# Kernel optimization log

Hardware: AMD Instinct MI355X
Metric: run time of the kernel (lower is better)

Reference implementation:

```python
import jax, jax.numpy as jnp
import numpy as np

B, NP, P, DIM = 128, 64, 128, 512
DST, DCONV, DEPTH = 16, 4, 2
DIN = 2 * DIM          # expand * dim
DTR = DIM // 16        # dt_rank
NCLS = 32


def setup_inputs() -> dict:
    key = jax.random.key(0)
    ks = jax.random.split(key, 12)
    r = lambda k, shape, s=0.02: jax.random.normal(k, shape, jnp.float32) * s
    A_log = jnp.log(jnp.arange(1, DST + 1, dtype=jnp.float32))  # S4D-real init
    return {
        "series": jax.random.normal(ks[0], (B, NP * P), jnp.float32),
        "seg_w": r(ks[1], (NP, P, DIM)),
        "seg_b": jnp.zeros((NP, DIM), jnp.float32),
        "ln_g": jnp.ones((NP, DIM), jnp.float32),
        "ln_b": jnp.zeros((NP, DIM), jnp.float32),
        "in_proj_w": r(ks[2], (DEPTH, 2 * DIN, DIM)),
        "conv_w": r(ks[3], (DEPTH, DIN, DCONV), 0.1),
        "conv_b": jnp.zeros((DEPTH, DIN), jnp.float32),
        "x_proj_w": r(ks[4], (DEPTH, DTR + 2 * DST, DIN)),
        "dt_proj_w": r(ks[5], (DEPTH, DIN, DTR), 0.1),
        "dt_proj_b": r(ks[6], (DEPTH, DIN), 0.5) - 4.0,  # small softplus(dt)
        "A_log": jnp.tile(A_log, (DEPTH, DIN, 1)),
        "D": jnp.ones((DEPTH, DIN), jnp.float32),
        "out_proj_w": r(ks[7], (DEPTH, DIM, DIN)),
        "head_ln_g": jnp.ones((NP * DIM,), jnp.float32),
        "head_ln_b": jnp.zeros((NP * DIM,), jnp.float32),
        "head_w": r(ks[8], (NCLS, NP * DIM)),
        "head_b": jnp.zeros((NCLS,), jnp.float32),
    }


def _layernorm(x, g, b, eps=1e-5):
    mu = x.mean(-1, keepdims=True)
    var = x.var(-1, keepdims=True)
    return (x - mu) / jnp.sqrt(var + eps) * g + b


def _mamba_block(x, wi, cw, cb, wx, wdt, bdt, A_log, Dp, wo):
    # x: [b, l, DIM]
    b, l, _ = x.shape
    xz = jnp.einsum('bld,ed->ble', x, wi)            # [b, l, 2*DIN]
    u, z = jnp.split(xz, 2, axis=-1)
    # depthwise causal conv1d (kernel DCONV, left pad DCONV-1)
    up = jnp.pad(u, ((0, 0), (DCONV - 1, 0), (0, 0)))
    uc = sum(up[:, k:k + l, :] * cw[:, k] for k in range(DCONV)) + cb
    uc = jax.nn.silu(uc)
    x_dbl = jnp.einsum('bld,ed->ble', uc, wx)        # [b, l, DTR+2*DST]
    dt, Bm, Cm = jnp.split(x_dbl, [DTR, DTR + DST], axis=-1)
    delta = jax.nn.softplus(jnp.einsum('blr,dr->bld', dt, wdt) + bdt)  # [b,l,DIN]
    A = -jnp.exp(A_log)                               # [DIN, DST]

    def step(h, inp):
        d_t, B_t, C_t, u_t = inp                      # [b,DIN],[b,DST],[b,DST],[b,DIN]
        dA = jnp.exp(d_t[:, :, None] * A)             # [b, DIN, DST]
        h = dA * h + (d_t * u_t)[:, :, None] * B_t[:, None, :]
        y = jnp.einsum('bdn,bn->bd', h, C_t)
        return h, y

    xs = (delta.transpose(1, 0, 2), Bm.transpose(1, 0, 2),
          Cm.transpose(1, 0, 2), uc.transpose(1, 0, 2))
    h0 = jnp.zeros((b, DIN, DST), x.dtype)
    _, ys = jax.lax.scan(step, h0, xs)                # [l, b, DIN]
    y = ys.transpose(1, 0, 2) + uc * Dp
    y = y * jax.nn.silu(z)
    return jnp.einsum('bld,ed->ble', y, wo)           # [b, l, DIM]


def _forward(series, seg_w, seg_b, ln_g, ln_b, in_proj_w, conv_w, conv_b,
             x_proj_w, dt_proj_w, dt_proj_b, A_log, D, out_proj_w,
             head_ln_g, head_ln_b, head_w, head_b):
    b = series.shape[0]
    x = series.reshape(b, NP, P)                      # equal-size pathway split
    x = jnp.einsum('bnp,npd->bnd', x, seg_w) + seg_b  # per-pathway Linear
    x = _layernorm(x, ln_g, ln_b)                     # per-pathway LayerNorm
    for i in range(DEPTH):                            # stacked Mamba (no residual)
        x = _mamba_block(x, in_proj_w[i], conv_w[i], conv_b[i], x_proj_w[i],
                         dt_proj_w[i], dt_proj_b[i], A_log[i], D[i], out_proj_w[i])
    x = x.reshape(b, NP * DIM)
    x = _layernorm(x, head_ln_g, head_ln_b)
    return x @ head_w.T + head_b


def reference(series, seg_w, seg_b, ln_g, ln_b, in_proj_w, conv_w, conv_b,
              x_proj_w, dt_proj_w, dt_proj_b, A_log, D, out_proj_w,
              head_ln_g, head_ln_b, head_w, head_b):
    return _forward(series, seg_w, seg_b, ln_g, ln_b, in_proj_w, conv_w, conv_b,
                    x_proj_w, dt_proj_w, dt_proj_b, A_log, D, out_proj_w,
                    head_ln_g, head_ln_b, head_w, head_b)
```

## Files before the change

### kernel.cpp

```cpp
#include <hip/hip_runtime.h>

typedef unsigned short u16;
typedef unsigned int   u32;
typedef __attribute__((ext_vector_type(8))) short short8;
typedef __attribute__((ext_vector_type(4))) float floatx4;

static __device__ __forceinline__ float silu_f(float x){
  return x / (1.f + __expf(-x));
}
static __device__ __forceinline__ float bfu2f(u16 u){
  union { u32 i; float f; } v; v.i = ((u32)u) << 16; return v.f;
}
static __device__ __forceinline__ u16 f2bfu(float f){
  union { float f; u32 i; } v; v.f = f;
  u32 x = v.i;
  u32 r = (x + 0x7fffu + ((x >> 16) & 1u)) >> 16;
  return (u16)r;
}
static __device__ __forceinline__ float softplus_f(float v){
  return fmaxf(v, 0.f) + log1pf(__expf(-fabsf(v)));
}

constexpr int cB = 128, cNP = 64, cP = 128, cDIM = 512, cDIN = 1024;
constexpr int cDST = 16, cDTR = 32, cNCLS = 32;
constexpr int cBL = cB * cNP;
constexpr int cXZ = 2 * cDIN;

__global__ __launch_bounds__(256) void k_f2bf(
    const float* __restrict__ src, u16* __restrict__ dst)
{
  const int i = (blockIdx.x * 256 + threadIdx.x) * 4;
  float4 v = *(const float4*)(src + i);
  ushort4 o;
  o.x = f2bfu(v.x); o.y = f2bfu(v.y); o.z = f2bfu(v.z); o.w = f2bfu(v.w);
  *(ushort4*)(dst + i) = o;
}

__global__ __launch_bounds__(256) void k_segT(
    const float* __restrict__ src, u16* __restrict__ dst)
{
  const int n = blockIdx.z;
  const int p0 = blockIdx.x * 32;
  const int d0 = blockIdx.y * 32;
  const int tx = threadIdx.x & 31;
  const int ty = threadIdx.x >> 5;
  __shared__ float t[32][33];
#pragma unroll
  for (int r = 0; r < 4; ++r)
    t[ty + r * 8][tx] = src[(size_t)n * (cP * cDIM) + (p0 + ty + r * 8) * cDIM + d0 + tx];
  __syncthreads();
#pragma unroll
  for (int r = 0; r < 4; ++r)
    dst[(size_t)n * (cDIM * cP) + (d0 + ty + r * 8) * cP + p0 + tx] =
        f2bfu(t[tx][ty + r * 8]);
}

template<bool AF32, int EPI>
__global__ __launch_bounds__(256) void k_gemm_mfma(
    const void* __restrict__ Av, int lda,
    const u16* __restrict__ W,
    float* __restrict__ C, int ldc,
    u16* __restrict__ Cb, int ldcb,
    const float* __restrict__ bias,
    int K, long azs, long wzs, long czs)
{
  constexpr int LDT = 40;
  __shared__ __align__(16) u16 As[128 * LDT];
  __shared__ __align__(16) u16 Ws[128 * LDT];

  const int bz = blockIdx.z;
  const u16* Wz = W + (size_t)bz * wzs;

  const int tid = threadIdx.x;
  const int bm = blockIdx.x * 128;
  const int bn = blockIdx.y * 128;
  const int wave = tid >> 6;
  const int lane = tid & 63;
  const int wm = (wave & 1) * 64;
  const int wn = (wave >> 1) * 64;
  const int l15 = lane & 15;
  const int quad = lane >> 4;

  floatx4 acc[4][4];
#pragma unroll
  for (int i = 0; i < 4; ++i)
#pragma unroll
    for (int j = 0; j < 4; ++j) acc[i][j] = (floatx4){0.f, 0.f, 0.f, 0.f};

  const int r0 = tid >> 2;
  const int c0 = (tid & 3) * 8;

  const float* Af = (const float*)Av + (AF32 ? (size_t)bz * azs : 0);
  const u16*   Ab = (const u16*)Av + (AF32 ? 0 : (size_t)bz * azs);

  float4 fa0, fb0, fa1, fb1;
  short8 ra0, ra1, rw0, rw1;

  if constexpr (AF32) {
    const float* p0 = Af + (size_t)(bm + r0) * lda + c0;
    const float* p1 = Af + (size_t)(bm + r0 + 64) * lda + c0;
    fa0 = *(const float4*)p0; fb0 = *(const float4*)(p0 + 4);
    fa1 = *(const float4*)p1; fb1 = *(const float4*)(p1 + 4);
  } else {
    ra0 = *(const short8*)(Ab + (size_t)(bm + r0)      * lda + c0);
    ra1 = *(const short8*)(Ab + (size_t)(bm + r0 + 64) * lda + c0);
  }
  rw0 = *(const short8*)(Wz + (size_t)(bn + r0)      * K + c0);
  rw1 = *(const short8*)(Wz + (size_t)(bn + r0 + 64) * K + c0);

  for (int k0 = 0; k0 < K; k0 += 32) {
    if constexpr (AF32) {
      short8 s0, s1;
      s0[0] = (short)f2bfu(fa0.x); s0[1] = (short)f2bfu(fa0.y);
      s0[2] = (short)f2bfu(fa0.z); s0[3] = (short)f2bfu(fa0.w);
      s0[4] = (short)f2bfu(fb0.x); s0[5] = (short)f2bfu(fb0.y);
      s0[6] = (short)f2bfu(fb0.z); s0[7] = (short)f2bfu(fb0.w);
      s1[0] = (short)f2bfu(fa1.x); s1[1] = (short)f2bfu(fa1.y);
      s1[2] = (short)f2bfu(fa1.z); s1[3] = (short)f2bfu(fa1.w);
      s1[4] = (short)f2bfu(fb1.x); s1[5] = (short)f2bfu(fb1.y);
      s1[6] = (short)f2bfu(fb1.z); s1[7] = (short)f2bfu(fb1.w);
      *(short8*)&As[r0 * LDT + c0] = s0;
      *(short8*)&As[(r0 + 64) * LDT + c0] = s1;
    } else {
      *(short8*)&As[r0 * LDT + c0] = ra0;
      *(short8*)&As[(r0 + 64) * LDT + c0] = ra1;
    }
    *(short8*)&Ws[r0 * LDT + c0] = rw0;
    *(short8*)&Ws[(r0 + 64) * LDT + c0] = rw1;
    __syncthreads();

    const int kn = k0 + 32;
    if (kn < K) {
      if constexpr (AF32) {
        const float* p0 = Af + (size_t)(bm + r0) * lda + kn + c0;
        const float* p1 = Af + (size_t)(bm + r0 + 64) * lda + kn + c0;
        fa0 = *(const float4*)p0; fb0 = *(const float4*)(p0 + 4);
        fa1 = *(const float4*)p1; fb1 = *(const float4*)(p1 + 4);
      } else {
        ra0 = *(const short8*)(Ab + (size_t)(bm + r0)      * lda + kn + c0);
        ra1 = *(const short8*)(Ab + (size_t)(bm + r0 + 64) * lda + kn + c0);
      }
      rw0 = *(const short8*)(Wz + (size_t)(bn + r0)      * K + kn + c0);
      rw1 = *(const short8*)(Wz + (size_t)(bn + r0 + 64) * K + kn + c0);
    }

    short8 af[4], bf[4];
#pragma unroll
    for (int i = 0; i < 4; ++i)
      af[i] = *(const short8*)&As[(wm + i * 16 + l15) * LDT + quad * 8];
#pragma unroll
    for (int j = 0; j < 4; ++j)
      bf[j] = *(const short8*)&Ws[(wn + j * 16 + l15) * LDT + quad * 8];
#pragma unroll
    for (int i = 0; i < 4; ++i)
#pragma unroll
      for (int j = 0; j < 4; ++j)
        acc[i][j] = __builtin_amdgcn_mfma_f32_16x16x32_bf16(
            af[i], bf[j], acc[i][j], 0, 0, 0);
    __syncthreads();
  }

#pragma unroll
  for (int i = 0; i < 4; ++i) {
    const int m0 = bm + wm + i * 16 + quad * 4;
#pragma unroll
    for (int j = 0; j < 4; ++j) {
      const int n = bn + wn + j * 16 + l15;
      if constexpr (EPI == 1) {
        const float bs = bias[n];
#pragma unroll
        for (int r = 0; r < 4; ++r)
          Cb[(size_t)(m0 + r) * ldcb + n + bz * czs] =
              f2bfu(softplus_f(acc[i][j][r] + bs));
      } else {
        if (C) {
#pragma unroll
          for (int r = 0; r < 4; ++r)
            C[(size_t)(m0 + r) * ldc + n + bz * czs] = acc[i][j][r];
        }
        if (Cb) {
#pragma unroll
          for (int r = 0; r < 4; ++r)
            Cb[(size_t)(m0 + r) * ldcb + n + bz * czs] = f2bfu(acc[i][j][r]);
        }
      }
    }
  }
}

__global__ __launch_bounds__(256) void k_ln(
    const float* __restrict__ xs, const float* __restrict__ sb,
    const float* __restrict__ ln_g, const float* __restrict__ ln_b,
    u16* __restrict__ x0b)
{
  const int tid = threadIdx.x;
  const int r = blockIdx.x * 4 + (tid >> 6);
  const int lane = tid & 63;
  const int d = lane * 8;
  const int n = r & 63;

  const float* row = xs + (size_t)r * cDIM + d;
  float4 a = *(const float4*)row;
  float4 b = *(const float4*)(row + 4);
  const float* sbp = sb + n * cDIM + d;
  float4 s0 = *(const float4*)sbp;
  float4 s1 = *(const float4*)(sbp + 4);
  a.x += s0.x; a.y += s0.y; a.z += s0.z; a.w += s0.w;
  b.x += s1.x; b.y += s1.y; b.z += s1.z; b.w += s1.w;

  float s  = a.x + a.y + a.z + a.w + b.x + b.y + b.z + b.w;
  float s2 = a.x*a.x + a.y*a.y + a.z*a.z + a.w*a.w
           + b.x*b.x + b.y*b.y + b.z*b.z + b.w*b.w;
#pragma unroll
  for (int m = 1; m < 64; m <<= 1) {
    s  += __shfl_xor(s,  m, 64);
    s2 += __shfl_xor(s2, m, 64);
  }
  const float mu = s * (1.f / cDIM);
  const float var = s2 * (1.f / cDIM) - mu * mu;
  const float rstd = rsqrtf(var + 1e-5f);

  const float* g = ln_g + n * cDIM + d;
  const float* be = ln_b + n * cDIM + d;
  float4 g0 = *(const float4*)g, g1 = *(const float4*)(g + 4);
  float4 b0 = *(const float4*)be, b1 = *(const float4*)(be + 4);
  ushort4 o0, o1;
  o0.x = f2bfu((a.x - mu) * rstd * g0.x + b0.x);
  o0.y = f2bfu((a.y - mu) * rstd * g0.y + b0.y);
  o0.z = f2bfu((a.z - mu) * rstd * g0.z + b0.z);
  o0.w = f2bfu((a.w - mu) * rstd * g0.w + b0.w);
  o1.x = f2bfu((b.x - mu) * rstd * g1.x + b1.x);
  o1.y = f2bfu((b.y - mu) * rstd * g1.y + b1.y);
  o1.z = f2bfu((b.z - mu) * rstd * g1.z + b1.z);
  o1.w = f2bfu((b.w - mu) * rstd * g1.w + b1.w);
  *(ushort4*)(x0b + (size_t)r * cDIM + d) = o0;
  *(ushort4*)(x0b + (size_t)r * cDIM + d + 4) = o1;
}

__global__ __launch_bounds__(256) void k_conv(
    const u16* __restrict__ xz16, const float* __restrict__ cw,
    const float* __restrict__ cb, u16* __restrict__ uc)
{
  const int t = blockIdx.x * 256 + threadIdx.x;
  const int b = t >> 10;
  const int d = t & 1023;
  const float w0 = cw[d * 4 + 0], w1 = cw[d * 4 + 1];
  const float w2 = cw[d * 4 + 2], w3 = cw[d * 4 + 3];
  const float bias = cb[d];
  const u16* src = xz16 + (size_t)b * cNP * cXZ + d;
  u16* dst = uc + (size_t)b * cNP * cDIN + d;

  float u0 = 0.f, u1 = 0.f, u2 = 0.f;
  float cur[8];
#pragma unroll
  for (int i = 0; i < 8; ++i) cur[i] = bfu2f(src[(size_t)i * cXZ]);

  for (int c = 0; c < 8; ++c) {
    float nxt[8];
    if (c < 7) {
#pragma unroll
      for (int i = 0; i < 8; ++i)
        nxt[i] = bfu2f(src[(size_t)((c + 1) * 8 + i) * cXZ]);
    }
    u16 o[8];
#pragma unroll
    for (int i = 0; i < 8; ++i) {
      float v = w0 * u0 + w1 * u1 + w2 * u2 + w3 * cur[i] + bias;
      o[i] = f2bfu(silu_f(v));
      u0 = u1; u1 = u2; u2 = cur[i];
    }
#pragma unroll
    for (int i = 0; i < 8; ++i) dst[(size_t)(c * 8 + i) * cDIN] = o[i];
    if (c < 7) {
#pragma unroll
      for (int i = 0; i < 8; ++i) cur[i] = nxt[i];
    }
  }
}

__global__ __launch_bounds__(128) void k_xproj(
    const u16* __restrict__ A, const u16* __restrict__ W,
    float* __restrict__ xpart)
{
  constexpr int LDT = 40;
  __shared__ __align__(16) u16 As[128 * LDT];
  __shared__ __align__(16) u16 Ws[64 * LDT];

  const int tid = threadIdx.x;
  const int bm = blockIdx.x * 128;
  const int kbase = blockIdx.y * 256;
  const int wave = tid >> 6;
  const int lane = tid & 63;
  const int wm = wave * 64;
  const int l15 = lane & 15;
  const int quad = lane >> 4;

  floatx4 acc[4][4];
#pragma unroll
  for (int i = 0; i < 4; ++i)
#pragma unroll
    for (int j = 0; j < 4; ++j) acc[i][j] = (floatx4){0.f, 0.f, 0.f, 0.f};

  short8 rA[4], rW[2];
#pragma unroll
  for (int it = 0; it < 4; ++it) {
    int idx = tid + it * 128, row = idx >> 2, cc = (idx & 3) * 8;
    rA[it] = *(const short8*)(A + (size_t)(bm + row) * cDIN + kbase + cc);
  }
#pragma unroll
  for (int it = 0; it < 2; ++it) {
    int idx = tid + it * 128, row = idx >> 2, cc = (idx & 3) * 8;
    rW[it] = *(const short8*)(W + (size_t)row * cDIN + kbase + cc);
  }

  for (int kk = 0; kk < 256; kk += 32) {
#pragma unroll
    for (int it = 0; it < 4; ++it) {
      int idx = tid + it * 128, row = idx >> 2, cc = (idx & 3) * 8;
      *(short8*)&As[row * LDT + cc] = rA[it];
    }
#pragma unroll
    for (int it = 0; it < 2; ++it) {
      int idx = tid + it * 128, row = idx >> 2, cc = (idx & 3) * 8;
      *(short8*)&Ws[row * LDT + cc] = rW[it];
    }
    __syncthreads();

    if (kk + 32 < 256) {
      const int k0 = kbase + kk + 32;
#pragma unroll
      for (int it = 0; it < 4; ++it) {
        int idx = tid + it * 128, row = idx >> 2, cc = (idx & 3) * 8;
        rA[it] = *(const short8*)(A + (size_t)(bm + row) * cDIN + k0 + cc);
      }
#pragma unroll
      for (int it = 0; it < 2; ++it) {
        int idx = tid + it * 128, row = idx >> 2, cc = (idx & 3) * 8;
        rW[it] = *(const short8*)(W + (size_t)row * cDIN + k0 + cc);
      }
    }

    short8 af[4], bf[4];
#pragma unroll
    for (int i = 0; i < 4; ++i)
      af[i] = *(const short8*)&As[(wm + i * 16 + l15) * LDT + quad * 8];
#pragma unroll
    for (int j = 0; j < 4; ++j)
      bf[j] = *(const short8*)&Ws[(j * 16 + l15) * LDT + quad * 8];
#pragma unroll
    for (int i = 0; i < 4; ++i)
#pragma unroll
      for (int j = 0; j < 4; ++j)
        acc[i][j] = __builtin_amdgcn_mfma_f32_16x16x32_bf16(
            af[i], bf[j], acc[i][j], 0, 0, 0);
    __syncthreads();
  }

  float* out = xpart + (size_t)blockIdx.y * cBL * 64;
#pragma unroll
  for (int i = 0; i < 4; ++i) {
    const int m0 = bm + wm + i * 16 + quad * 4;
#pragma unroll
    for (int j = 0; j < 4; ++j) {
      const int n = j * 16 + l15;
#pragma unroll
      for (int r = 0; r < 4; ++r)
        out[(size_t)(m0 + r) * 64 + n] = acc[i][j][r];
    }
  }
}

__global__ __launch_bounds__(256) void k_xred(
    const float* __restrict__ xpart, float* __restrict__ C,
    u16* __restrict__ Cb)
{
  const int i = (blockIdx.x * 256 + threadIdx.x) * 4;
  float4 s = *(const float4*)(xpart + i);
#pragma unroll
  for (int k = 1; k < 4; ++k) {
    float4 v = *(const float4*)(xpart + (size_t)k * cBL * 64 + i);
    s.x += v.x; s.y += v.y; s.z += v.z; s.w += v.w;
  }
  *(float4*)(C + i) = s;
  ushort4 o;
  o.x = f2bfu(s.x); o.y = f2bfu(s.y); o.z = f2bfu(s.z); o.w = f2bfu(s.w);
  *(ushort4*)(Cb + i) = o;
}

__global__ __launch_bounds__(256) void k_scan(
    const u16* __restrict__ xz16, u16* __restrict__ uc,
    const float* __restrict__ xdbl, const float* __restrict__ A_log,
    const float* __restrict__ Dp)
{
  const int b = blockIdx.x;
  const int tid = threadIdx.x;
  const int d = blockIdx.y * 256 + tid;

  __shared__ float sBC[cNP][32];
  {
    const float4* src = (const float4*)xdbl;
    for (int i = tid; i < cNP * 8; i += 256) {
      int l = i >> 3, q = i & 7;
      *(float4*)&sBC[l][q * 4] = src[(size_t)(b * cNP + l) * 16 + 8 + q];
    }
  }

  float A[cDST];
  {
    const float4* ap = (const float4*)(A_log + (size_t)d * cDST);
#pragma unroll
    for (int q = 0; q < 4; ++q) {
      float4 w = ap[q];
      A[q*4+0] = -__expf(w.x); A[q*4+1] = -__expf(w.y);
      A[q*4+2] = -__expf(w.z); A[q*4+3] = -__expf(w.w);
    }
  }
  float h[cDST];
#pragma unroll
  for (int n = 0; n < cDST; ++n) h[n] = 0.f;
  const float Dv = Dp[d];
  __syncthreads();

  const u16* dsrc = xz16 + d;
  const u16* zsrc = xz16 + cDIN + d;
  u16* usrc = uc + d;
  const size_t rb = (size_t)b * cNP;

  float dvc[8], zvc[8], uvc[8];
#pragma unroll
  for (int i = 0; i < 8; ++i) {
    dvc[i] = bfu2f(dsrc[(rb + i) * cXZ]);
    zvc[i] = bfu2f(zsrc[(rb + i) * cXZ]);
    uvc[i] = bfu2f(usrc[(rb + i) * cDIN]);
  }

  for (int c = 0; c < 8; ++c) {
    float dvn[8], zvn[8], uvn[8];
    if (c < 7) {
#pragma unroll
      for (int i = 0; i < 8; ++i) {
        const size_t row = rb + (c + 1) * 8 + i;
        dvn[i] = bfu2f(dsrc[row * cXZ]);
        zvn[i] = bfu2f(zsrc[row * cXZ]);
        uvn[i] = bfu2f(usrc[row * cDIN]);
      }
    }
    u16 yo[8];
#pragma unroll
    for (int i = 0; i < 8; ++i) {
      const int l = c * 8 + i;
      const float dv = dvc[i], zv = zvc[i], uv = uvc[i];
      const float du = dv * uv;
      float y = 0.f;
#pragma unroll
      for (int n = 0; n < cDST; ++n) {
        float dA = __expf(dv * A[n]);
        h[n] = dA * h[n] + du * sBC[l][n];
        y += h[n] * sBC[l][16 + n];
      }
      y = (y + uv * Dv) * silu_f(zv);
      yo[i] = f2bfu(y);
    }
#pragma unroll
    for (int i = 0; i < 8; ++i)
      usrc[(rb + c * 8 + i) * cDIN] = yo[i];
    if (c < 7) {
#pragma unroll
      for (int i = 0; i < 8; ++i) {
        dvc[i] = dvn[i]; zvc[i] = zvn[i]; uvc[i] = uvn[i];
      }
    }
  }
}

__global__ __launch_bounds__(256) void k_hstats1(
    const float* __restrict__ x, float* __restrict__ pst)
{
  const int b = blockIdx.x;
  const int chunk = blockIdx.y;
  const int tid = threadIdx.x;
  const float4* r4 = (const float4*)(x + (size_t)b * (cNP * cDIM) + chunk * 4096);
  float4 v = r4[tid];
  float4 w = r4[tid + 256];
  float4 u = r4[tid + 512];
  float4 t = r4[tid + 768];
  float s  = v.x + v.y + v.z + v.w + w.x + w.y + w.z + w.w
           + u.x + u.y + u.z + u.w + t.x + t.y + t.z + t.w;
  float s2 = v.x*v.x + v.y*v.y + v.z*v.z + v.w*v.w
           + w.x*w.x + w.y*w.y + w.z*w.z + w.w*w.w
           + u.x*u.x + u.y*u.y + u.z*u.z + u.w*u.w
           + t.x*t.x + t.y*t.y + t.z*t.z + t.w*t.w;
  __shared__ float red[512];
  red[tid] = s; red[256 + tid] = s2;
  __syncthreads();
  for (int st = 128; st > 0; st >>= 1) {
    if (tid < st) { red[tid] += red[tid + st]; red[256+tid] += red[256+tid+st]; }
    __syncthreads();
  }
  if (tid == 0) {
    pst[(b * 8 + chunk) * 2]     = red[0];
    pst[(b * 8 + chunk) * 2 + 1] = red[256];
  }
}

__global__ __launch_bounds__(128) void k_hstats2(
    const float* __restrict__ pst, float* __restrict__ stats)
{
  const int b = threadIdx.x;
  float s = 0.f, s2 = 0.f;
#pragma unroll
  for (int c = 0; c < 8; ++c) {
    s  += pst[(b * 8 + c) * 2];
    s2 += pst[(b * 8 + c) * 2 + 1];
  }
  const float mu = s * (1.f / (cNP * cDIM));
  const float var = s2 * (1.f / (cNP * cDIM)) - mu * mu;
  stats[2 * b]     = mu;
  stats[2 * b + 1] = rsqrtf(var + 1e-5f);
}

__global__ __launch_bounds__(256) void k_head1(
    const float* __restrict__ x, const float* __restrict__ stats,
    const float* __restrict__ hg, const float* __restrict__ hb,
    const u16* __restrict__ hwb, float* __restrict__ hpart)
{
  const int b = blockIdx.x;
  const int chunk = blockIdx.y;
  const int tid = threadIdx.x;
  const float mu = stats[2 * b], rstd = stats[2 * b + 1];
  const float* row = x + (size_t)b * (cNP * cDIM);
  const int k0 = chunk * 2048;

  float acc[cNCLS];
#pragma unroll
  for (int c = 0; c < cNCLS; ++c) acc[c] = 0.f;

#pragma unroll
  for (int it = 0; it < 4; ++it) {
    const int i0 = k0 + it * 512 + tid * 2;
    float xn0 = (row[i0]     - mu) * rstd * hg[i0]     + hb[i0];
    float xn1 = (row[i0 + 1] - mu) * rstd * hg[i0 + 1] + hb[i0 + 1];
#pragma unroll
    for (int c = 0; c < cNCLS; ++c) {
      u32 w2 = *(const u32*)(hwb + (size_t)c * (cNP * cDIM) + i0);
      acc[c] += xn0 * bfu2f((u16)(w2 & 0xffffu)) + xn1 * bfu2f((u16)(w2 >> 16));
    }
  }

  __shared__ float sred[cNCLS * 257];
#pragma unroll
  for (int c = 0; c < cNCLS; ++c) sred[c * 257 + tid] = acc[c];
  __syncthreads();
  if (tid < cNCLS * 8) {
    const int c = tid >> 3, p = tid & 7;
    float s = 0.f;
#pragma unroll
    for (int i = 0; i < 32; ++i) s += sred[c * 257 + p * 32 + i];
    s += __shfl_xor(s, 1, 64);
    s += __shfl_xor(s, 2, 64);
    s += __shfl_xor(s, 4, 64);
    if (p == 0) hpart[(size_t)(b * 16 + chunk) * cNCLS + c] = s;
  }
}

__global__ __launch_bounds__(64) void k_head2(
    const float* __restrict__ hpart, const float* __restrict__ hbias,
    float* __restrict__ out)
{
  const int b = blockIdx.x;
  const int c = threadIdx.x;
  if (c < cNCLS) {
    float s = 0.f;
#pragma unroll
    for (int k = 0; k < 16; ++k)
      s += hpart[(size_t)(b * 16 + k) * cNCLS + c];
    out[b * cNCLS + c] = s + hbias[c];
  }
}

extern "C" void kernel_launch(void* const* d_in, const int* in_sizes, int n_in,
                              void* d_out, int out_size, void* d_ws, size_t ws_size,
                              hipStream_t stream)
{
  (void)in_sizes; (void)n_in; (void)out_size; (void)ws_size;

  const float* series    = (const float*)d_in[0];
  const float* seg_w     = (const float*)d_in[1];
  const float* seg_b     = (const float*)d_in[2];
  const float* ln_g      = (const float*)d_in[3];
  const float* ln_b      = (const float*)d_in[4];
  const float* in_proj_w = (const float*)d_in[5];
  const float* conv_w    = (const float*)d_in[6];
  const float* conv_b    = (const float*)d_in[7];
  const float* x_proj_w  = (const float*)d_in[8];
  const float* dt_proj_w = (const float*)d_in[9];
  const float* dt_proj_b = (const float*)d_in[10];
  const float* A_log     = (const float*)d_in[11];
  const float* Dp        = (const float*)d_in[12];
  const float* out_proj_w= (const float*)d_in[13];
  const float* head_ln_g = (const float*)d_in[14];
  const float* head_ln_b = (const float*)d_in[15];
  const float* head_w    = (const float*)d_in[16];
  const float* head_b    = (const float*)d_in[17];

  u16*   xz16   = (u16*)d_ws;
  float* x0     = (float*)(xz16 + (size_t)cBL * cXZ);
  float* xsegf  = x0;
  float* xdbl   = x0 + (size_t)cBL * cDIM;
  float* stats  = xdbl + (size_t)cBL * 64;
  float* pst    = stats + 256;
  float* hpart  = pst + 128 * 8 * 2;
  u16*   x0b    = (u16*)(hpart + 128 * 16 * 32);
  u16*   wib    = x0b + (size_t)cBL * cDIM;
  u16*   wob    = wib + (size_t)2 * (2*cDIN) * cDIM;
  u16*   wdtb   = wob + (size_t)2 * cDIM * cDIN;
  u16*   wxb    = wdtb + (size_t)2 * cDIN * cDTR;
  u16*   xdbl16 = wxb + (size_t)2 * 64 * cDIN;
  u16*   wsegT  = xdbl16 + (size_t)cBL * 64;
  u16*   ucb16  = wsegT + (size_t)cNP * cDIM * cP;
  u16*   hwb    = ucb16 + (size_t)cBL * cDIN;
  float* xpart  = (float*)x0b;

  k_f2bf<<<(2 * (2*cDIN) * cDIM) / 1024, 256, 0, stream>>>(in_proj_w, wib);
  k_f2bf<<<(2 * cDIM * cDIN) / 1024, 256, 0, stream>>>(out_proj_w, wob);
  k_f2bf<<<(2 * cDIN * cDTR) / 1024, 256, 0, stream>>>(dt_proj_w, wdtb);
  k_f2bf<<<(2 * 64 * cDIN) / 1024, 256, 0, stream>>>(x_proj_w, wxb);
  k_f2bf<<<(cNCLS * cNP * cDIM) / 1024, 256, 0, stream>>>(head_w, hwb);
  k_segT<<<dim3(cP/32, cDIM/32, cNP), 256, 0, stream>>>(seg_w, wsegT);

  k_gemm_mfma<true,0><<<dim3(1, cDIM/128, cNP), 256, 0, stream>>>(
      series, cNP * cP, wsegT, xsegf, cNP * cDIM, (u16*)nullptr, 0,
      nullptr, cP, (long)cP, (long)cDIM * cP, (long)cDIM);
  k_ln<<<cBL / 4, 256, 0, stream>>>(xsegf, seg_b, ln_g, ln_b, x0b);

  for (int dep = 0; dep < 2; ++dep) {
    const u16*   wi  = wib  + (size_t)dep * (2*cDIN) * cDIM;
    const u16*   wo  = wob  + (size_t)dep * cDIM * cDIN;
    const u16*   wdt = wdtb + (size_t)dep * cDIN * cDTR;
    const u16*   wx  = wxb  + (size_t)dep * 64 * cDIN;
    const float* cwd = conv_w     + (size_t)dep * cDIN * 4;
    const float* cbd = conv_b     + (size_t)dep * cDIN;
    const float* bdt = dt_proj_b  + (size_t)dep * cDIN;
    const float* Ald = A_log      + (size_t)dep * cDIN * cDST;
    const float* Dd  = Dp         + (size_t)dep * cDIN;

    k_gemm_mfma<false,0><<<dim3(cBL/128, (2*cDIN)/128), 256, 0, stream>>>(
        x0b, cDIM, wi, (float*)nullptr, 0, xz16, cXZ, nullptr, cDIM, 0, 0, 0);
    k_conv<<<(cB * cDIN) / 256, 256, 0, stream>>>(xz16, cwd, cbd, ucb16);
    k_xproj<<<dim3(cBL / 128, 4), 128, 0, stream>>>(ucb16, wx, xpart);
    k_xred<<<(cBL * 64) / 1024, 256, 0, stream>>>(xpart, xdbl, xdbl16);
    k_gemm_mfma<false,1><<<dim3(cBL/128, cDIN/128), 256, 0, stream>>>(
        xdbl16, 64, wdt, (float*)nullptr, 0, xz16, cXZ, bdt, cDTR, 0, 0, 0);
    k_scan<<<dim3(cB, 4), 256, 0, stream>>>(xz16, ucb16, xdbl, Ald, Dd);
    k_gemm_mfma<false,0><<<dim3(cBL/128, cDIM/128), 256, 0, stream>>>(
        ucb16, cDIN, wo,
        dep ? x0 : (float*)nullptr, cDIM,
        dep ? (u16*)nullptr : x0b, cDIM,
        nullptr, cDIN, 0, 0, 0);
  }

  k_hstats1<<<dim3(cB, 8), 256, 0, stream>>>(x0, pst);
  k_hstats2<<<1, 128, 0, stream>>>(pst, stats);
  k_head1<<<dim3(cB, 16), 256, 0, stream>>>(x0, stats, head_ln_g, head_ln_b,
                                            hwb, hpart);
  k_head2<<<cB, 64, 0, stream>>>(hpart, head_b, (float*)d_out);
}
```

Baseline: 438.6 us.

## Fuse causal conv into in_proj GEMM epilogue and use geometric exp in scan

The in_proj GEMM gains an epilogue mode that stages the u half of each tile in LDS and applies the depthwise causal conv plus SiLU directly, removing the separate conv kernel and its global read of u. The scan kernel detects at runtime whether A follows the S4D-real geometric pattern and, if so, replaces 16 exponentials per step with one exp and repeated multiplication. The fused epilogue adds 32KB of shared memory per block, which may cut occupancy. The power chain adds small rounding drift compared with computing each exp directly.

```diff
diff --git a/kernel.cpp b/kernel.cpp
--- a/kernel.cpp
+++ b/kernel.cpp
@@ -62,11 +62,14 @@
     float* __restrict__ C, int ldc,
     u16* __restrict__ Cb, int ldcb,
     const float* __restrict__ bias,
-    int K, long azs, long wzs, long czs)
+    int K, long azs, long wzs, long czs,
+    const float* __restrict__ cwp, const float* __restrict__ cbp,
+    u16* __restrict__ ucp)
 {
   constexpr int LDT = 40;
   __shared__ __align__(16) u16 As[128 * LDT];
   __shared__ __align__(16) u16 Ws[128 * LDT];
+  __shared__ __align__(16) u16 sU[(EPI == 2) ? 128 * 128 : 1];
 
   const int bz = blockIdx.z;
   const u16* Wz = W + (size_t)bz * wzs;
@@ -160,6 +163,40 @@
     __syncthreads();
   }
 
+  if constexpr (EPI == 2) {
+    if (bn < cDIN) {
+#pragma unroll
+      for (int i = 0; i < 4; ++i) {
+        const int mi = wm + i * 16 + quad * 4;
+#pragma unroll
+        for (int j = 0; j < 4; ++j) {
+          const int nj = wn + j * 16 + l15;
+#pragma unroll
+          for (int r = 0; r < 4; ++r)
+            sU[(mi + r) * 128 + nj] = f2bfu(acc[i][j][r]);
+        }
+      }
+      __syncthreads();
+      const int c = tid & 127;
+      const int s = tid >> 7;
+      const int b = (bm >> 6) + s;
+      const int d = bn + c;
+      const float w0 = cwp[d * 4 + 0], w1 = cwp[d * 4 + 1];
+      const float w2 = cwp[d * 4 + 2], w3 = cwp[d * 4 + 3];
+      const float cbias = cbp[d];
+      u16* dst = ucp + (size_t)b * cNP * cDIN + d;
+      float u0 = 0.f, u1 = 0.f, u2 = 0.f;
+#pragma unroll 8
+      for (int l = 0; l < cNP; ++l) {
+        float u3 = bfu2f(sU[(s * 64 + l) * 128 + c]);
+        float v = w0 * u0 + w1 * u1 + w2 * u2 + w3 * u3 + cbias;
+        dst[(size_t)l * cDIN] = f2bfu(silu_f(v));
+        u0 = u1; u1 = u2; u2 = u3;
+      }
+      return;
+    }
+  }
+
 #pragma unroll
   for (int i = 0; i < 4; ++i) {
     const int m0 = bm + wm + i * 16 + quad * 4;
@@ -237,47 +274,6 @@
   *(ushort4*)(x0b + (size_t)r * cDIM + d + 4) = o1;
 }
 
-__global__ __launch_bounds__(256) void k_conv(
-    const u16* __restrict__ xz16, const float* __restrict__ cw,
-    const float* __restrict__ cb, u16* __restrict__ uc)
-{
-  const int t = blockIdx.x * 256 + threadIdx.x;
-  const int b = t >> 10;
-  const int d = t & 1023;
-  const float w0 = cw[d * 4 + 0], w1 = cw[d * 4 + 1];
-  const float w2 = cw[d * 4 + 2], w3 = cw[d * 4 + 3];
-  const float bias = cb[d];
-  const u16* src = xz16 + (size_t)b * cNP * cXZ + d;
-  u16* dst = uc + (size_t)b * cNP * cDIN + d;
-
-  float u0 = 0.f, u1 = 0.f, u2 = 0.f;
-  float cur[8];
-#pragma unroll
-  for (int i = 0; i < 8; ++i) cur[i] = bfu2f(src[(size_t)i * cXZ]);
-
-  for (int c = 0; c < 8; ++c) {
-    float nxt[8];
-    if (c < 7) {
-#pragma unroll
-      for (int i = 0; i < 8; ++i)
-        nxt[i] = bfu2f(src[(size_t)((c + 1) * 8 + i) * cXZ]);
-    }
-    u16 o[8];
-#pragma unroll
-    for (int i = 0; i < 8; ++i) {
-      float v = w0 * u0 + w1 * u1 + w2 * u2 + w3 * cur[i] + bias;
-      o[i] = f2bfu(silu_f(v));
-      u0 = u1; u1 = u2; u2 = cur[i];
-    }
-#pragma unroll
-    for (int i = 0; i < 8; ++i) dst[(size_t)(c * 8 + i) * cDIN] = o[i];
-    if (c < 7) {
-#pragma unroll
-      for (int i = 0; i < 8; ++i) cur[i] = nxt[i];
-    }
-  }
-}
-
 __global__ __launch_bounds__(128) void k_xproj(
     const u16* __restrict__ A, const u16* __restrict__ W,
     float* __restrict__ xpart)
@@ -415,6 +411,12 @@
       A[q*4+2] = -__expf(w.z); A[q*4+3] = -__expf(w.w);
     }
   }
+  const float a1 = A[0];
+  bool geom = true;
+#pragma unroll
+  for (int n = 1; n < cDST; ++n)
+    geom = geom && (fabsf(A[n] - (float)(n + 1) * a1) <= 1e-4f * fabsf(A[n]));
+
   float h[cDST];
 #pragma unroll
   for (int n = 0; n < cDST; ++n) h[n] = 0.f;
@@ -434,40 +436,82 @@
     uvc[i] = bfu2f(usrc[(rb + i) * cDIN]);
   }
 
-  for (int c = 0; c < 8; ++c) {
-    float dvn[8], zvn[8], uvn[8];
-    if (c < 7) {
+  if (geom) {
+    for (int c = 0; c < 8; ++c) {
+      float dvn[8], zvn[8], uvn[8];
+      if (c < 7) {
+#pragma unroll
+        for (int i = 0; i < 8; ++i) {
+          const size_t row = rb + (c + 1) * 8 + i;
+          dvn[i] = bfu2f(dsrc[row * cXZ]);
+          zvn[i] = bfu2f(zsrc[row * cXZ]);
+          uvn[i] = bfu2f(usrc[row * cDIN]);
+        }
+      }
+      u16 yo[8];
 #pragma unroll
       for (int i = 0; i < 8; ++i) {
-        const size_t row = rb + (c + 1) * 8 + i;
-        dvn[i] = bfu2f(dsrc[row * cXZ]);
-        zvn[i] = bfu2f(zsrc[row * cXZ]);
-        uvn[i] = bfu2f(usrc[row * cDIN]);
-      }
-    }
-    u16 yo[8];
-#pragma unroll
-    for (int i = 0; i < 8; ++i) {
-      const int l = c * 8 + i;
-      const float dv = dvc[i], zv = zvc[i], uv = uvc[i];
-      const float du = dv * uv;
-      float y = 0.f;
-#pragma unroll
-      for (int n = 0; n < cDST; ++n) {
-        float dA = __expf(dv * A[n]);
-        h[n] = dA * h[n] + du * sBC[l][n];
-        y += h[n] * sBC[l][16 + n];
-      }
-      y = (y + uv * Dv) * silu_f(zv);
-      yo[i] = f2bfu(y);
-    }
-#pragma unroll
-    for (int i = 0; i < 8; ++i)
-      usrc[(rb + c * 8 + i) * cDIN] = yo[i];
-    if (c < 7) {
+        const int l = c * 8 + i;
+        const float dv = dvc[i], zv = zvc[i], uv = uvc[i];
+        const float du = dv * uv;
+        const float e1 = __expf(dv * a1);
+        float dA = e1;
+        float y = 0.f;
+#pragma unroll
+        for (int n = 0; n < cDST; ++n) {
+          h[n] = dA * h[n] + du * sBC[l][n];
+          y += h[n] * sBC[l][16 + n];
+          dA *= e1;
+        }
+        y = (y + uv * Dv) * silu_f(zv);
+        yo[i] = f2bfu(y);
+      }
+#pragma unroll
+      for (int i = 0; i < 8; ++i)
+        usrc[(rb + c * 8 + i) * cDIN] = yo[i];
+      if (c < 7) {
+#pragma unroll
+        for (int i = 0; i < 8; ++i) {
+          dvc[i] = dvn[i]; zvc[i] = zvn[i]; uvc[i] = uvn[i];
+        }
+      }
+    }
+  } else {
+    for (int c = 0; c < 8; ++c) {
+      float dvn[8], zvn[8], uvn[8];
+      if (c < 7) {
+#pragma unroll
+        for (int i = 0; i < 8; ++i) {
+          const size_t row = rb + (c + 1) * 8 + i;
+          dvn[i] = bfu2f(dsrc[row * cXZ]);
+          zvn[i] = bfu2f(zsrc[row * cXZ]);
+          uvn[i] = bfu2f(usrc[row * cDIN]);
+        }
+      }
+      u16 yo[8];
 #pragma unroll
       for (int i = 0; i < 8; ++i) {
-        dvc[i] = dvn[i]; zvc[i] = zvn[i]; uvc[i] = uvn[i];
+        const int l = c * 8 + i;
+        const float dv = dvc[i], zv = zvc[i], uv = uvc[i];
+        const float du = dv * uv;
+        float y = 0.f;
+#pragma unroll
+        for (int n = 0; n < cDST; ++n) {
+          float dA = __expf(dv * A[n]);
+          h[n] = dA * h[n] + du * sBC[l][n];
+          y += h[n] * sBC[l][16 + n];
+        }
+        y = (y + uv * Dv) * silu_f(zv);
+        yo[i] = f2bfu(y);
+      }
+#pragma unroll
+      for (int i = 0; i < 8; ++i)
+        usrc[(rb + c * 8 + i) * cDIN] = yo[i];
+      if (c < 7) {
+#pragma unroll
+        for (int i = 0; i < 8; ++i) {
+          dvc[i] = dvn[i]; zvc[i] = zvn[i]; uvc[i] = uvn[i];
+        }
       }
     }
   }
@@ -630,7 +674,8 @@
 
   k_gemm_mfma<true,0><<<dim3(1, cDIM/128, cNP), 256, 0, stream>>>(
       series, cNP * cP, wsegT, xsegf, cNP * cDIM, (u16*)nullptr, 0,
-      nullptr, cP, (long)cP, (long)cDIM * cP, (long)cDIM);
+      nullptr, cP, (long)cP, (long)cDIM * cP, (long)cDIM,
+      nullptr, nullptr, nullptr);
   k_ln<<<cBL / 4, 256, 0, stream>>>(xsegf, seg_b, ln_g, ln_b, x0b);
 
   for (int dep = 0; dep < 2; ++dep) {
@@ -644,19 +689,21 @@
     const float* Ald = A_log      + (size_t)dep * cDIN * cDST;
     const float* Dd  = Dp         + (size_t)dep * cDIN;
 
-    k_gemm_mfma<false,0><<<dim3(cBL/128, (2*cDIN)/128), 256, 0, stream>>>(
-        x0b, cDIM, wi, (float*)nullptr, 0, xz16, cXZ, nullptr, cDIM, 0, 0, 0);
-    k_conv<<<(cB * cDIN) / 256, 256, 0, stream>>>(xz16, cwd, cbd, ucb16);
+    k_gemm_mfma<false,2><<<dim3(cBL/128, (2*cDIN)/128), 256, 0, stream>>>(
+        x0b, cDIM, wi, (float*)nullptr, 0, xz16, cXZ, nullptr, cDIM, 0, 0, 0,
+        cwd, cbd, ucb16);
     k_xproj<<<dim3(cBL / 128, 4), 128, 0, stream>>>(ucb16, wx, xpart);
     k_xred<<<(cBL * 64) / 1024, 256, 0, stream>>>(xpart, xdbl, xdbl16);
     k_gemm_mfma<false,1><<<dim3(cBL/128, cDIN/128), 256, 0, stream>>>(
-        xdbl16, 64, wdt, (float*)nullptr, 0, xz16, cXZ, bdt, cDTR, 0, 0, 0);
+        xdbl16, 64, wdt, (float*)nullptr, 0, xz16, cXZ, bdt, cDTR, 0, 0, 0,
+        nullptr, nullptr, nullptr);
     k_scan<<<dim3(cB, 4), 256, 0, stream>>>(xz16, ucb16, xdbl, Ald, Dd);
     k_gemm_mfma<false,0><<<dim3(cBL/128, cDIM/128), 256, 0, stream>>>(
         ucb16, cDIN, wo,
         dep ? x0 : (float*)nullptr, cDIM,
         dep ? (u16*)nullptr : x0b, cDIM,
-        nullptr, cDIN, 0, 0, 0);
+        nullptr, cDIN, 0, 0, 0,
+        nullptr, nullptr, nullptr);
   }
 
   k_hstats1<<<dim3(cB, 8), 256, 0, stream>>>(x0, pst);
```

New measurement: 401.2 us. 1.09x faster.
